# Kernel tuning notes

Hardware: AMD Instinct MI355X
Metric: run time of the kernel (lower is better)

## Reference

```python
import jax, jax.numpy as jnp
import numpy as np

POOL_SIZE = 7
NUM_ROIS = 512


def setup_inputs() -> dict:
    key = jax.random.key(0)
    k1, k2 = jax.random.split(key)
    img = jax.random.normal(k1, (8, 200, 200, 256), dtype=jnp.float32)
    rois = jax.random.uniform(k2, (8, NUM_ROIS, 4), dtype=jnp.float32)  # normalized [y1,x1,y2,x2]
    return {"img": img, "rois": rois}


def _crop_and_resize(img, boxes, box_idx, crop):
    """TF tf.image.crop_and_resize (bilinear, extrapolation_value=0).
    img: [B,H,W,C]; boxes: [N,4] normalized [y1,x1,y2,x2]; box_idx: [N] int32.
    Returns [N, crop, crop, C]."""
    B, H, W, C = img.shape
    y1, x1, y2, x2 = boxes[:, 0], boxes[:, 1], boxes[:, 2], boxes[:, 3]
    i = jnp.arange(crop, dtype=img.dtype)
    # TF formula for crop>1: in_y = y1*(H-1) + i*(y2-y1)*(H-1)/(crop-1)
    ys = y1[:, None] * (H - 1) + i[None, :] * ((y2 - y1) * (H - 1) / (crop - 1))[:, None]  # [N,P]
    xs = x1[:, None] * (W - 1) + i[None, :] * ((x2 - x1) * (W - 1) / (crop - 1))[:, None]  # [N,P]

    valid_y = (ys >= 0) & (ys <= H - 1)
    valid_x = (xs >= 0) & (xs <= W - 1)

    y0f = jnp.floor(ys)
    x0f = jnp.floor(xs)
    fy = (ys - y0f)[:, :, None, None]   # [N,P,1,1]
    fx = (xs - x0f)[:, None, :, None]   # [N,1,P,1]

    y0 = jnp.clip(y0f.astype(jnp.int32), 0, H - 1)
    y1i = jnp.clip(y0 + 1, 0, H - 1)
    x0 = jnp.clip(x0f.astype(jnp.int32), 0, W - 1)
    x1i = jnp.clip(x0 + 1, 0, W - 1)

    b = box_idx[:, None, None]  # [N,1,1]
    # Four corner gathers, each [N,P,P,C]
    v00 = img[b, y0[:, :, None], x0[:, None, :]]
    v01 = img[b, y0[:, :, None], x1i[:, None, :]]
    v10 = img[b, y1i[:, :, None], x0[:, None, :]]
    v11 = img[b, y1i[:, :, None], x1i[:, None, :]]

    top = v00 + (v01 - v00) * fx
    bot = v10 + (v11 - v10) * fx
    out = top + (bot - top) * fy

    mask = (valid_y[:, :, None] & valid_x[:, None, :])[..., None]
    return jnp.where(mask, out, jnp.zeros((), dtype=img.dtype))


def reference(img, rois):
    B, H, W, C = img.shape
    boxes = rois.reshape(-1, 4)                      # [B*R, 4]
    n = boxes.shape[0]
    box_idx = jnp.arange(n, dtype=jnp.int32) // NUM_ROIS
    res = _crop_and_resize(img, boxes, box_idx, POOL_SIZE)
    return res.reshape(-1, NUM_ROIS, POOL_SIZE, POOL_SIZE, C)
```

## Files before the change

### kernel.cpp

```cpp
#include <hip/hip_runtime.h>

#define POOL 7
#define NROIS 512
#define IMG_H 200
#define IMG_W 200
#define IMG_C 256

__global__ __launch_bounds__(448) void roi_crop_resize_kernel(
    const float* __restrict__ img,
    const float* __restrict__ rois,
    float* __restrict__ out,
    int nBoxes, int doSwz)
{
    int n, py;
    if (doSwz) {
        const int xcd  = blockIdx.x & 7;
        const int slot = blockIdx.x >> 3;
        n  = (slot / POOL) * 8 + xcd;
        py = slot - (slot / POOL) * POOL;
    } else {
        n  = blockIdx.x / POOL;
        py = blockIdx.x - n * POOL;
    }

    const int tid = threadIdx.x;
    const int px = tid >> 6;
    const int c4 = (tid & 63) << 2;

    const float4 box = *(const float4*)(rois + (size_t)n * 4);
    const float by1 = box.x;
    const float bx1 = box.y;
    const float by2 = box.z;
    const float bx2 = box.w;
    const int b = n / NROIS;

    const float ys = by1 * (float)(IMG_H - 1)
                   + (float)py * ((by2 - by1) * (float)(IMG_H - 1) / (float)(POOL - 1));
    const float xs = bx1 * (float)(IMG_W - 1)
                   + (float)px * ((bx2 - bx1) * (float)(IMG_W - 1) / (float)(POOL - 1));

    const bool valid = (ys >= 0.0f) && (ys <= (float)(IMG_H - 1))
                    && (xs >= 0.0f) && (xs <= (float)(IMG_W - 1));

    float4 r = make_float4(0.f, 0.f, 0.f, 0.f);

    if (valid) {
        const float y0f = floorf(ys);
        const float x0f = floorf(xs);
        const float fy = ys - y0f;
        const float fx = xs - x0f;

        int y0 = (int)y0f; y0 = min(max(y0, 0), IMG_H - 1);
        const int y1i = min(y0 + 1, IMG_H - 1);
        int x0 = (int)x0f; x0 = min(max(x0, 0), IMG_W - 1);
        const int x1i = min(x0 + 1, IMG_W - 1);

        const size_t rowStride = (size_t)IMG_W * IMG_C;
        const size_t base = (size_t)b * IMG_H * rowStride + (size_t)c4;
        const float* p00 = img + base + (size_t)y0  * rowStride + (size_t)x0  * IMG_C;
        const float* p01 = img + base + (size_t)y0  * rowStride + (size_t)x1i * IMG_C;
        const float* p10 = img + base + (size_t)y1i * rowStride + (size_t)x0  * IMG_C;
        const float* p11 = img + base + (size_t)y1i * rowStride + (size_t)x1i * IMG_C;

        const float4 v00 = *(const float4*)p00;
        const float4 v01 = *(const float4*)p01;
        const float4 v10 = *(const float4*)p10;
        const float4 v11 = *(const float4*)p11;

        float tx, bx;
        tx = v00.x + (v01.x - v00.x) * fx;  bx = v10.x + (v11.x - v10.x) * fx;
        r.x = tx + (bx - tx) * fy;
        tx = v00.y + (v01.y - v00.y) * fx;  bx = v10.y + (v11.y - v10.y) * fx;
        r.y = tx + (bx - tx) * fy;
        tx = v00.z + (v01.z - v00.z) * fx;  bx = v10.z + (v11.z - v10.z) * fx;
        r.z = tx + (bx - tx) * fy;
        tx = v00.w + (v01.w - v00.w) * fx;  bx = v10.w + (v11.w - v10.w) * fx;
        r.w = tx + (bx - tx) * fy;
    }

    float* o = out + (((size_t)n * POOL + py) * POOL + px) * IMG_C + c4;
    __builtin_nontemporal_store(r.x, o + 0);
    __builtin_nontemporal_store(r.y, o + 1);
    __builtin_nontemporal_store(r.z, o + 2);
    __builtin_nontemporal_store(r.w, o + 3);
}

extern "C" void kernel_launch(void* const* d_in, const int* in_sizes, int n_in,
                              void* d_out, int out_size, void* d_ws, size_t ws_size,
                              hipStream_t stream) {
    const float* img  = (const float*)d_in[0];
    const float* rois = (const float*)d_in[1];
    float* out = (float*)d_out;

    const int nBoxes = in_sizes[1] / 4;
    const int grid = nBoxes * POOL;
    const int doSwz = (nBoxes % 8 == 0) ? 1 : 0;

    roi_crop_resize_kernel<<<grid, 448, 0, stream>>>(img, rois, out, nBoxes, doSwz);
}
```

Before: 491.0 us.

## Sort ROIs by vertical center per batch to improve cache locality of gathers

Adds a small kernel that histogram-sorts boxes within each batch image by their y-center into 128 bins and writes a permutation to workspace. The main kernel then handles boxes in that order, so neighbouring blocks read nearby image rows, aiming for better L2/MALL reuse of the bilinear corner reads. The XCD swizzle is removed, and the change adds an extra kernel launch plus one indirect load per block.

```diff
diff --git a/kernel.cpp b/kernel.cpp
--- a/kernel.cpp
+++ b/kernel.cpp
@@ -5,23 +5,46 @@
 #define IMG_H 200
 #define IMG_W 200
 #define IMG_C 256
+#define NBINS 128
+
+__global__ __launch_bounds__(NROIS) void sort_boxes_kernel(
+    const float* __restrict__ rois, int* __restrict__ perm)
+{
+    __shared__ int hist[NBINS];
+    __shared__ int offs[NBINS];
+    const int b = blockIdx.x;
+    const int t = threadIdx.x;
+    if (t < NBINS) hist[t] = 0;
+    __syncthreads();
+
+    const int n = b * NROIS + t;
+    const float y1 = rois[(size_t)n * 4 + 0];
+    const float y2 = rois[(size_t)n * 4 + 2];
+    const float yc = 0.5f * (y1 + y2);
+    int bin = (int)(yc * (float)NBINS);
+    bin = min(max(bin, 0), NBINS - 1);
+    const int rank = atomicAdd(&hist[bin], 1);
+    __syncthreads();
+
+    if (t == 0) {
+        int acc = 0;
+        for (int i = 0; i < NBINS; ++i) { offs[i] = acc; acc += hist[i]; }
+    }
+    __syncthreads();
+
+    perm[b * NROIS + offs[bin] + rank] = n;
+}
 
 __global__ __launch_bounds__(448) void roi_crop_resize_kernel(
     const float* __restrict__ img,
     const float* __restrict__ rois,
-    float* __restrict__ out,
-    int nBoxes, int doSwz)
+    const int* __restrict__ perm,
+    float* __restrict__ out)
 {
-    int n, py;
-    if (doSwz) {
-        const int xcd  = blockIdx.x & 7;
-        const int slot = blockIdx.x >> 3;
-        n  = (slot / POOL) * 8 + xcd;
-        py = slot - (slot / POOL) * POOL;
-    } else {
-        n  = blockIdx.x / POOL;
-        py = blockIdx.x - n * POOL;
-    }
+    const int blk = blockIdx.x;
+    const int s  = blk / POOL;
+    const int py = blk - s * POOL;
+    const int n  = perm[s];
 
     const int tid = threadIdx.x;
     const int px = tid >> 6;
@@ -91,10 +114,13 @@
     const float* img  = (const float*)d_in[0];
     const float* rois = (const float*)d_in[1];
     float* out = (float*)d_out;
+    int*   perm = (int*)d_ws;
 
-    const int nBoxes = in_sizes[1] / 4;
+    const int nBoxes   = in_sizes[1] / 4;
+    const int nBatches = nBoxes / NROIS;
+
+    sort_boxes_kernel<<<nBatches, NROIS, 0, stream>>>(rois, perm);
+
     const int grid = nBoxes * POOL;
-    const int doSwz = (nBoxes % 8 == 0) ? 1 : 0;
-
-    roi_crop_resize_kernel<<<grid, 448, 0, stream>>>(img, rois, out, nBoxes, doSwz);
+    roi_crop_resize_kernel<<<grid, 448, 0, stream>>>(img, rois, perm, out);
 }
```

New measurement: 487.6 us. No clear change (-0.7%).
